# Performance work log

Hardware: AMD Instinct MI355X
Metric: run time of the kernel (lower is better)

The kernel has to match this reference:

```python
import jax, jax.numpy as jnp
import numpy as np

L = 4          # num_blocks
D = 256        # emb_dim
H = 8          # num_heads
DH = D         # per-head dim == emb_dim (module quirk: inner_dim = emb_dim * num_heads)
INNER = D * H  # 2048
M = 1024       # mlp_dim
EPS = 1e-5
SCALE = D ** (-0.5)


def layernorm(x, g, b):
    mu = jnp.mean(x, axis=-1, keepdims=True)
    var = jnp.mean(jnp.square(x - mu), axis=-1, keepdims=True)
    return (x - mu) * jax.lax.rsqrt(var + EPS) * g + b


def setup_inputs() -> dict:
    key = jax.random.key(0)
    ks = jax.random.split(key, 12)
    B, N = 8, 1024
    s = lambda fan: 1.0 / np.sqrt(fan)
    return {
        "inputs": jax.random.normal(ks[0], (B, N, D), dtype=jnp.float32),
        "ln1_g": jnp.ones((L, D), jnp.float32),
        "ln1_b": jnp.zeros((L, D), jnp.float32),
        "w_qkv": jax.random.normal(ks[1], (L, D, 3 * INNER), jnp.float32) * s(D),
        "w_proj": jax.random.normal(ks[2], (L, INNER, D), jnp.float32) * s(INNER),
        "b_proj": jnp.zeros((L, D), jnp.float32),
        "ln2_g": jnp.ones((L, D), jnp.float32),
        "ln2_b": jnp.zeros((L, D), jnp.float32),
        "w1": jax.random.normal(ks[3], (L, D, M), jnp.float32) * s(D),
        "b1": jnp.zeros((L, M), jnp.float32),
        "w2": jax.random.normal(ks[4], (L, M, D), jnp.float32) * s(M),
        "b2": jnp.zeros((L, D), jnp.float32),
    }


def attention(x, w_qkv, w_proj, b_proj):
    B, N, _ = x.shape
    qkv = x @ w_qkv                                  # [B, N, 3*INNER]
    q, k, v = jnp.split(qkv, 3, axis=-1)
    reshape = lambda t: t.reshape(B, N, H, DH).transpose(0, 2, 1, 3)  # b h n d
    q, k, v = reshape(q), reshape(k), reshape(v)
    dots = jnp.einsum("bhnd,bhmd->bhnm", q, k) * SCALE
    attn = jax.nn.softmax(dots, axis=-1)
    out = jnp.einsum("bhnm,bhmd->bhnd", attn, v)     # [B, H, N, DH]
    out = out.transpose(0, 2, 1, 3).reshape(B, N, INNER)
    return out @ w_proj + b_proj


def reference(inputs, ln1_g, ln1_b, w_qkv, w_proj, b_proj, ln2_g, ln2_b, w1, b1, w2, b2):
    x = inputs
    for l in range(L):
        # pre-LN multi-head attention + residual
        h = layernorm(x, ln1_g[l], ln1_b[l])
        x = x + attention(h, w_qkv[l], w_proj[l], b_proj[l])
        # pre-LN GELU MLP + residual (exact erf GELU, matching nn.GELU default)
        h = layernorm(x, ln2_g[l], ln2_b[l])
        h = jax.nn.gelu(h @ w1[l] + b1[l], approximate=False)
        x = x + (h @ w2[l] + b2[l])
    return x
```

## Files before the change

kernel.cpp:

```cpp
#include <hip/hip_runtime.h>
#include <math.h>

#define L_ 4
#define D_ 256
#define H_ 8
#define INNER_ 2048
#define M_ 1024
#define B_ 8
#define N_ 1024
#define R_ (B_ * N_)
#define QS_ 6144

constexpr float EPS_ = 1e-5f;
constexpr float SCALE_ = 0.0625f;

using f16 = _Float16;
typedef _Float16 f16x8 __attribute__((ext_vector_type(8)));
typedef float f32x4 __attribute__((ext_vector_type(4)));

__device__ __forceinline__ float gelu_f(float x) {
    return 0.5f * x * (1.0f + erff(x * 0.70710678118654752f));
}

__global__ __launch_bounds__(256)
void ln_kernel(const float* __restrict__ x, const float* __restrict__ g,
               const float* __restrict__ b, f16* __restrict__ out) {
    const int row = blockIdx.x;
    const int t = threadIdx.x;
    const int wave = t >> 6, lane = t & 63;
    __shared__ float red[8];

    const float v = x[(size_t)row * D_ + t];

    float s = v;
    #pragma unroll
    for (int o = 32; o; o >>= 1) s += __shfl_down(s, o);
    if (lane == 0) red[wave] = s;
    __syncthreads();
    const float mean = (red[0] + red[1] + red[2] + red[3]) * (1.0f / 256.0f);

    const float d = v - mean;
    float s2 = d * d;
    #pragma unroll
    for (int o = 32; o; o >>= 1) s2 += __shfl_down(s2, o);
    if (lane == 0) red[4 + wave] = s2;
    __syncthreads();
    const float var = (red[4] + red[5] + red[6] + red[7]) * (1.0f / 256.0f);

    out[(size_t)row * D_ + t] = (f16)(d * rsqrtf(var + EPS_) * g[t] + b[t]);
}

__global__ __launch_bounds__(256)
void transpose_w(const float* __restrict__ W, f16* __restrict__ Wt, int K, int N) {
    __shared__ float tile[64][68];
    const int n0 = blockIdx.x * 64, k0 = blockIdx.y * 64;
    const float* Wl = W + (size_t)blockIdx.z * K * N;
    f16* Wtl = Wt + (size_t)blockIdx.z * K * N;
    const int t = threadIdx.x;

    #pragma unroll
    for (int j = 0; j < 4; ++j) {
        const int li = t + 256 * j;
        const int r = li >> 4, c4 = (li & 15) * 4;
        const float4 v = *reinterpret_cast<const float4*>(&Wl[(size_t)(k0 + r) * N + n0 + c4]);
        tile[r][c4] = v.x; tile[r][c4 + 1] = v.y; tile[r][c4 + 2] = v.z; tile[r][c4 + 3] = v.w;
    }
    __syncthreads();
    #pragma unroll
    for (int j = 0; j < 2; ++j) {
        const int li = t + 256 * j;
        const int n = li >> 3, c8 = (li & 7) * 8;
        f16 tmp[8];
        #pragma unroll
        for (int e = 0; e < 8; ++e) tmp[e] = (f16)tile[c8 + e][n];
        *reinterpret_cast<uint4*>(&Wtl[(size_t)(n0 + n) * K + k0 + c8]) =
            *reinterpret_cast<const uint4*>(tmp);
    }
}

__global__ __launch_bounds__(256)
void transpose_v(const f16* __restrict__ qkv, f16* __restrict__ Vt) {
    __shared__ f16 tile[64][72];
    const int n0 = blockIdx.x * 64;
    const int d0 = blockIdx.y * 64;
    const int b = blockIdx.z;
    const int t = threadIdx.x;
    const f16* Vg = qkv + (size_t)b * N_ * QS_ + 4096;

    #pragma unroll
    for (int j = 0; j < 2; ++j) {
        const int li = t + 256 * j;
        const int r = li >> 3, c8 = (li & 7) * 8;
        *reinterpret_cast<uint4*>(&tile[r][c8]) =
            *reinterpret_cast<const uint4*>(&Vg[(size_t)(n0 + r) * QS_ + d0 + c8]);
    }
    __syncthreads();
    #pragma unroll
    for (int j = 0; j < 2; ++j) {
        const int li = t + 256 * j;
        const int dr = li >> 3, c8 = (li & 7) * 8;
        f16 tmp[8];
        #pragma unroll
        for (int e = 0; e < 8; ++e) tmp[e] = tile[c8 + e][dr];
        *reinterpret_cast<uint4*>(&Vt[((size_t)b * INNER_ + d0 + dr) * N_ + n0 + c8]) =
            *reinterpret_cast<const uint4*>(tmp);
    }
}

template <int WM, int WN, bool BIAS, bool RES, bool GELU, bool OUTF16>
__global__ __launch_bounds__(256)
void gemm_f16(const f16* __restrict__ A, int lda, const f16* __restrict__ Wt,
              const float* __restrict__ bias, f16* __restrict__ Cf16,
              float* __restrict__ Cf32, int ldc, int K) {
    constexpr int BM = 2 * WM, BN = 2 * WN, MI = WM / 16, NI = WN / 16;
    __shared__ uint4 As[BM * 8];
    __shared__ uint4 Bs[BN * 8];

    const int t = threadIdx.x;
    const int lane = t & 63, w = t >> 6;
    const int wr = w >> 1, wc = w & 1;
    const int row0 = blockIdx.y * BM, col0 = blockIdx.x * BN;
    const int l15 = lane & 15, l4 = lane >> 4;

    f32x4 acc[MI][NI];
    #pragma unroll
    for (int mi = 0; mi < MI; ++mi)
        #pragma unroll
        for (int ni = 0; ni < NI; ++ni) acc[mi][ni] = (f32x4){0.f, 0.f, 0.f, 0.f};

    for (int k0 = 0; k0 < K; k0 += 64) {
        #pragma unroll
        for (int j = 0; j < BM / 32; ++j) {
            const int ci = t + 256 * j, r = ci >> 3, c = ci & 7;
            As[r * 8 + (c ^ (r & 7))] =
                *reinterpret_cast<const uint4*>(&A[(size_t)(row0 + r) * lda + k0 + c * 8]);
        }
        #pragma unroll
        for (int j = 0; j < BN / 32; ++j) {
            const int ci = t + 256 * j, r = ci >> 3, c = ci & 7;
            Bs[r * 8 + (c ^ (r & 7))] =
                *reinterpret_cast<const uint4*>(&Wt[(size_t)(col0 + r) * K + k0 + c * 8]);
        }
        __syncthreads();

        #pragma unroll
        for (int tk = 0; tk < 2; ++tk) {
            f16x8 af[MI], bf[NI];
            #pragma unroll
            for (int mi = 0; mi < MI; ++mi) {
                const int r = wr * WM + mi * 16 + l15;
                af[mi] = *reinterpret_cast<const f16x8*>(&As[r * 8 + ((tk * 4 + l4) ^ (r & 7))]);
            }
            #pragma unroll
            for (int ni = 0; ni < NI; ++ni) {
                const int r = wc * WN + ni * 16 + l15;
                bf[ni] = *reinterpret_cast<const f16x8*>(&Bs[r * 8 + ((tk * 4 + l4) ^ (r & 7))]);
            }
            #pragma unroll
            for (int mi = 0; mi < MI; ++mi)
                #pragma unroll
                for (int ni = 0; ni < NI; ++ni)
                    acc[mi][ni] = __builtin_amdgcn_mfma_f32_16x16x32_f16(
                        af[mi], bf[ni], acc[mi][ni], 0, 0, 0);
        }
        __syncthreads();
    }

    #pragma unroll
    for (int mi = 0; mi < MI; ++mi) {
        #pragma unroll
        for (int ni = 0; ni < NI; ++ni) {
            const int col = col0 + wc * WN + ni * 16 + l15;
            float bv = 0.f;
            if constexpr (BIAS) bv = bias[col];
            #pragma unroll
            for (int r = 0; r < 4; ++r) {
                const size_t row = row0 + wr * WM + mi * 16 + l4 * 4 + r;
                float v = acc[mi][ni][r] + bv;
                if constexpr (GELU) v = gelu_f(v);
                if constexpr (OUTF16) {
                    Cf16[row * ldc + col] = (f16)v;
                } else {
                    float* p = &Cf32[row * ldc + col];
                    *p = RES ? (*p + v) : v;
                }
            }
        }
    }
}

__global__ __launch_bounds__(512, 1)
void attn_f16(f16* __restrict__ qkv, const f16* __restrict__ Vt) {
    __shared__ uint4 lds[9216];
    f16* Ps = (f16*)(lds + 8192);

    const int t = threadIdx.x, lane = t & 63, w = t >> 6;
    const int l15 = lane & 15, l4 = lane >> 4;
    const int lin = blockIdx.x;
    const int hh = lin & 7;
    const int q0 = ((lin >> 3) & 7) << 7;
    const int b = lin >> 6;

    f16* Qg = qkv + (size_t)b * N_ * QS_ + hh * 256;
    const f16* Kg = Qg + 2048;
    const f16* Vtg = Vt + ((size_t)b * INNER_ + hh * 256) * N_;

    uint4 qreg[8];
    #pragma unroll
    for (int j = 0; j < 8; ++j) {
        const int ci = t + 512 * j, r = ci >> 5, c = ci & 31;
        qreg[j] = *reinterpret_cast<const uint4*>(&Qg[(size_t)(q0 + r) * QS_ + c * 8]);
    }
    uint4 kreg[4], vreg[4];
    #pragma unroll
    for (int j = 0; j < 4; ++j) {
        const int ci = t + 512 * j, r = ci >> 5, c = ci & 31;
        kreg[j] = *reinterpret_cast<const uint4*>(&Kg[(size_t)r * QS_ + c * 8]);
    }
    #pragma unroll
    for (int j = 0; j < 4; ++j) {
        const int ci = t + 512 * j, r = ci >> 3, c = ci & 7;
        vreg[j] = *reinterpret_cast<const uint4*>(&Vtg[(size_t)r * N_ + c * 8]);
    }
    #pragma unroll
    for (int j = 0; j < 8; ++j) {
        const int ci = t + 512 * j, r = ci >> 5, c = ci & 31;
        lds[r * 32 + (c ^ (r & 7))] = qreg[j];
    }
    __syncthreads();
    f16x8 qf[8];
    {
        const int r = w * 16 + l15;
        #pragma unroll
        for (int tk = 0; tk < 8; ++tk)
            qf[tk] = *reinterpret_cast<const f16x8*>(&lds[r * 32 + ((tk * 4 + l4) ^ (r & 7))]);
    }
    __syncthreads();

    float m_run[4] = {-INFINITY, -INFINITY, -INFINITY, -INFINITY};
    float l_run[4] = {0.f, 0.f, 0.f, 0.f};
    f32x4 outf[16];
    #pragma unroll
    for (int f = 0; f < 16; ++f) outf[f] = (f32x4){0.f, 0.f, 0.f, 0.f};

    for (int kt = 0; kt < 16; ++kt) {
        uint4* Kc = (kt & 1) ? (lds + 2048) : lds;
        uint4* Vc = (kt & 1) ? (lds + 6144) : (lds + 4096);

        #pragma unroll
        for (int j = 0; j < 4; ++j) {
            const int ci = t + 512 * j, r = ci >> 5, c = ci & 31;
            Kc[r * 32 + (c ^ (r & 7))] = kreg[j];
        }
        #pragma unroll
        for (int j = 0; j < 4; ++j) {
            const int ci = t + 512 * j, r = ci >> 3, c = ci & 7;
            Vc[r * 8 + (c ^ (r & 7))] = vreg[j];
        }
        if (kt < 15) {
            const int kv0n = (kt + 1) * 64;
            #pragma unroll
            for (int j = 0; j < 4; ++j) {
                const int ci = t + 512 * j, r = ci >> 5, c = ci & 31;
                kreg[j] = *reinterpret_cast<const uint4*>(
                    &Kg[(size_t)(kv0n + r) * QS_ + c * 8]);
            }
            #pragma unroll
            for (int j = 0; j < 4; ++j) {
                const int ci = t + 512 * j, r = ci >> 3, c = ci & 7;
                vreg[j] = *reinterpret_cast<const uint4*>(
                    &Vtg[(size_t)r * N_ + kv0n + c * 8]);
            }
        }
        __syncthreads();

        f32x4 sf[4];
        #pragma unroll
        for (int nf = 0; nf < 4; ++nf) sf[nf] = (f32x4){0.f, 0.f, 0.f, 0.f};
        __builtin_amdgcn_s_setprio(1);
        #pragma unroll
        for (int tk = 0; tk < 8; ++tk) {
            #pragma unroll
            for (int nf = 0; nf < 4; ++nf) {
                const int r = nf * 16 + l15;
                const f16x8 bf =
                    *reinterpret_cast<const f16x8*>(&Kc[r * 32 + ((tk * 4 + l4) ^ (r & 7))]);
                sf[nf] = __builtin_amdgcn_mfma_f32_16x16x32_f16(qf[tk], bf, sf[nf], 0, 0, 0);
            }
        }
        __builtin_amdgcn_s_setprio(0);

        float mx[4], al[4], ps[4], p[4][4];
        #pragma unroll
        for (int r = 0; r < 4; ++r) {
            float v0 = sf[0][r] * SCALE_, v1 = sf[1][r] * SCALE_;
            float v2 = sf[2][r] * SCALE_, v3 = sf[3][r] * SCALE_;
            p[0][r] = v0; p[1][r] = v1; p[2][r] = v2; p[3][r] = v3;
            mx[r] = fmaxf(fmaxf(v0, v1), fmaxf(v2, v3));
        }
        #pragma unroll
        for (int off = 1; off < 16; off <<= 1)
            #pragma unroll
            for (int r = 0; r < 4; ++r) mx[r] = fmaxf(mx[r], __shfl_xor(mx[r], off));
        #pragma unroll
        for (int r = 0; r < 4; ++r) {
            const float nm = fmaxf(m_run[r], mx[r]);
            al[r] = __expf(m_run[r] - nm);
            m_run[r] = nm;
            float sum = 0.f;
            #pragma unroll
            for (int nf = 0; nf < 4; ++nf) {
                p[nf][r] = __expf(p[nf][r] - nm);
                sum += p[nf][r];
            }
            ps[r] = sum;
        }
        #pragma unroll
        for (int off = 1; off < 16; off <<= 1)
            #pragma unroll
            for (int r = 0; r < 4; ++r) ps[r] += __shfl_xor(ps[r], off);
        #pragma unroll
        for (int r = 0; r < 4; ++r) {
            l_run[r] = l_run[r] * al[r] + ps[r];
            const int q = w * 16 + l4 * 4 + r;
            #pragma unroll
            for (int nf = 0; nf < 4; ++nf) {
                const int kv = nf * 16 + l15;
                Ps[q * 64 + (kv ^ ((q & 7) << 3))] = (f16)p[nf][r];
            }
        }
        #pragma unroll
        for (int f = 0; f < 16; ++f)
            #pragma unroll
            for (int r = 0; r < 4; ++r) outf[f][r] *= al[r];

        __builtin_amdgcn_s_setprio(1);
        #pragma unroll
        for (int tk = 0; tk < 2; ++tk) {
            const int rq = w * 16 + l15;
            const int c = tk * 4 + l4;
            const f16x8 pa =
                *reinterpret_cast<const f16x8*>(&Ps[rq * 64 + ((c ^ (rq & 7)) * 8)]);
            #pragma unroll
            for (int f = 0; f < 16; ++f) {
                const int d = f * 16 + l15;
                const f16x8 vf = *reinterpret_cast<const f16x8*>(&Vc[d * 8 + (c ^ (d & 7))]);
                outf[f] = __builtin_amdgcn_mfma_f32_16x16x32_f16(pa, vf, outf[f], 0, 0, 0);
            }
        }
        __builtin_amdgcn_s_setprio(0);
    }

    __syncthreads();
    constexpr int OST = 272;
    f16* Os = (f16*)lds;
    float inv[4];
    #pragma unroll
    for (int r = 0; r < 4; ++r) inv[r] = 1.0f / l_run[r];
    #pragma unroll
    for (int f = 0; f < 16; ++f) {
        const int d = f * 16 + l15;
        #pragma unroll
        for (int r = 0; r < 4; ++r) {
            const int q = w * 16 + l4 * 4 + r;
            Os[q * OST + d] = (f16)(outf[f][r] * inv[r]);
        }
    }
    __syncthreads();
    #pragma unroll
    for (int j = 0; j < 8; ++j) {
        const int id = t + 512 * j;
        const int row = id >> 5, cc = id & 31;
        *reinterpret_cast<uint4*>(&Qg[(size_t)(q0 + row) * QS_ + cc * 8]) =
            *reinterpret_cast<const uint4*>(&Os[row * OST + cc * 8]);
    }
}

extern "C" void kernel_launch(void* const* d_in, const int* in_sizes, int n_in,
                              void* d_out, int out_size, void* d_ws, size_t ws_size,
                              hipStream_t stream) {
    (void)in_sizes; (void)n_in; (void)out_size;

    const float* inputs = (const float*)d_in[0];
    const float* ln1_g  = (const float*)d_in[1];
    const float* ln1_b  = (const float*)d_in[2];
    const float* w_qkv  = (const float*)d_in[3];
    const float* w_proj = (const float*)d_in[4];
    const float* b_proj = (const float*)d_in[5];
    const float* ln2_g  = (const float*)d_in[6];
    const float* ln2_b  = (const float*)d_in[7];
    const float* w1     = (const float*)d_in[8];
    const float* b1     = (const float*)d_in[9];
    const float* w2     = (const float*)d_in[10];
    const float* b2     = (const float*)d_in[11];

    float* x = (float*)d_out;

    f16* ws = (f16*)d_ws;
    const size_t SZ_WQKV = (size_t)L_ * D_ * 3 * INNER_;
    const size_t SZ_WPRJ = (size_t)L_ * INNER_ * D_;
    const size_t SZ_W1   = (size_t)L_ * D_ * M_;
    const size_t SZ_W2   = (size_t)L_ * M_ * D_;
    const size_t SZ_H    = (size_t)R_ * D_;
    f16* wt_qkv = ws;
    f16* wt_prj = wt_qkv + SZ_WQKV;
    f16* wt1    = wt_prj + SZ_WPRJ;
    f16* wt2    = wt1 + SZ_W1;
    f16* h      = wt2 + SZ_W2;
    f16* qc     = h + SZ_H;

    const size_t fixed = SZ_WQKV + SZ_WPRJ + SZ_W1 + SZ_W2 + SZ_H;
    int nch = 1;
    while (nch < 8 &&
           2 * (fixed + ((size_t)R_ / nch) * (QS_ + INNER_)) > ws_size)
        nch *= 2;
    const int CB = B_ / nch;
    const int CR = R_ / nch;
    f16* vt = qc + (size_t)CR * QS_;

    hipMemcpyAsync(x, inputs, (size_t)R_ * D_ * sizeof(float),
                   hipMemcpyDeviceToDevice, stream);

    transpose_w<<<dim3(96, 4, L_), 256, 0, stream>>>(w_qkv, wt_qkv, D_, 3 * INNER_);
    transpose_w<<<dim3(4, 32, L_), 256, 0, stream>>>(w_proj, wt_prj, INNER_, D_);
    transpose_w<<<dim3(16, 4, L_), 256, 0, stream>>>(w1, wt1, D_, M_);
    transpose_w<<<dim3(4, 16, L_), 256, 0, stream>>>(w2, wt2, M_, D_);

    for (int l = 0; l < L_; ++l) {
        ln_kernel<<<R_, 256, 0, stream>>>(x, ln1_g + l * D_, ln1_b + l * D_, h);

        for (int c = 0; c < nch; ++c) {
            const size_t r0 = (size_t)c * CR;
            gemm_f16<64, 64, false, false, false, true>
                <<<dim3(QS_ / 128, CR / 128), 256, 0, stream>>>(
                    h + r0 * D_, D_, wt_qkv + (size_t)l * D_ * 3 * INNER_,
                    nullptr, qc, nullptr, QS_, D_);

            transpose_v<<<dim3(16, 32, CB), 256, 0, stream>>>(qc, vt);

            attn_f16<<<(N_ / 128) * H_ * CB, 512, 0, stream>>>(qc, vt);

            gemm_f16<32, 32, true, true, false, false>
                <<<dim3(D_ / 64, CR / 64), 256, 0, stream>>>(
                    qc, QS_, wt_prj + (size_t)l * INNER_ * D_,
                    b_proj + l * D_, nullptr, x + r0 * D_, D_, INNER_);
        }

        ln_kernel<<<R_, 256, 0, stream>>>(x, ln2_g + l * D_, ln2_b + l * D_, h);

        for (int c = 0; c < nch; ++c) {
            const size_t r0 = (size_t)c * CR;
            f16* hid = qc;
            gemm_f16<64, 64, true, false, true, true>
                <<<dim3(M_ / 128, CR / 128), 256, 0, stream>>>(
                    h + r0 * D_, D_, wt1 + (size_t)l * D_ * M_,
                    b1 + l * M_, hid, nullptr, M_, D_);

            gemm_f16<32, 32, true, true, false, false>
                <<<dim3(D_ / 64, CR / 64), 256, 0, stream>>>(
                    hid, M_, wt2 + (size_t)l * M_ * D_,
                    b2 + l * D_, nullptr, x + r0 * D_, D_, M_);
        }
    }
}
```

Before: 1.654 ms.

## Restructure attention kernel with direct global-to-LDS loads and 2 m-tiles per wave

Rewrites the flash-attention kernel to use 256 threads with each wave handling two 16-row query tiles, sharing K fragments across both tiles. K/V tiles shrink to 32 keys and are streamed with global_load_lds directly into double-buffered LDS, replacing register staging. Row sums are computed with an MFMA against a ones vector instead of shuffle reductions. The launch bounds allow two blocks per CU for occupancy. The costs are twice as many loop iterations, each carrying a block-wide barrier, and roughly doubled accumulator register pressure.

```diff
diff --git a/kernel.cpp b/kernel.cpp
--- a/kernel.cpp
+++ b/kernel.cpp
@@ -20,6 +20,12 @@
 
 __device__ __forceinline__ float gelu_f(float x) {
     return 0.5f * x * (1.0f + erff(x * 0.70710678118654752f));
+}
+
+__device__ __forceinline__ void gll16(const f16* src, f16* dst) {
+    __builtin_amdgcn_global_load_lds(
+        (const __attribute__((address_space(1))) unsigned int*)src,
+        (__attribute__((address_space(3))) unsigned int*)dst, 16, 0, 0);
 }
 
 __global__ __launch_bounds__(256)
@@ -189,10 +195,10 @@
     }
 }
 
-__global__ __launch_bounds__(512, 1)
+__global__ __launch_bounds__(256, 2)
 void attn_f16(f16* __restrict__ qkv, const f16* __restrict__ Vt) {
-    __shared__ uint4 lds[9216];
-    f16* Ps = (f16*)(lds + 8192);
+    __shared__ alignas(16) f16 lds[36864];
+    f16* const Ps = lds + 32768;
 
     const int t = threadIdx.x, lane = t & 63, w = t >> 6;
     const int l15 = lane & 15, l4 = lane >> 4;
@@ -205,147 +211,166 @@
     const f16* Kg = Qg + 2048;
     const f16* Vtg = Vt + ((size_t)b * INNER_ + hh * 256) * N_;
 
-    uint4 qreg[8];
-    #pragma unroll
-    for (int j = 0; j < 8; ++j) {
-        const int ci = t + 512 * j, r = ci >> 5, c = ci & 31;
-        qreg[j] = *reinterpret_cast<const uint4*>(&Qg[(size_t)(q0 + r) * QS_ + c * 8]);
-    }
-    uint4 kreg[4], vreg[4];
-    #pragma unroll
-    for (int j = 0; j < 4; ++j) {
-        const int ci = t + 512 * j, r = ci >> 5, c = ci & 31;
-        kreg[j] = *reinterpret_cast<const uint4*>(&Kg[(size_t)r * QS_ + c * 8]);
-    }
-    #pragma unroll
-    for (int j = 0; j < 4; ++j) {
-        const int ci = t + 512 * j, r = ci >> 3, c = ci & 7;
-        vreg[j] = *reinterpret_cast<const uint4*>(&Vtg[(size_t)r * N_ + c * 8]);
-    }
-    #pragma unroll
-    for (int j = 0; j < 8; ++j) {
-        const int ci = t + 512 * j, r = ci >> 5, c = ci & 31;
-        lds[r * 32 + (c ^ (r & 7))] = qreg[j];
-    }
-    __syncthreads();
-    f16x8 qf[8];
+    #pragma unroll
+    for (int j = 0; j < 32; ++j) {
+        const int cb = (j * 4 + w) << 6;
+        const int ci = cb + lane;
+        const int r = ci >> 5, c = ci & 31;
+        gll16(Qg + (size_t)(q0 + r) * QS_ + ((c ^ (r & 7)) << 3), lds + cb * 8);
+    }
+    __syncthreads();
+    f16x8 qf[2][8];
+    #pragma unroll
+    for (int mi = 0; mi < 2; ++mi) {
+        const int q = w * 32 + mi * 16 + l15;
+        #pragma unroll
+        for (int tk = 0; tk < 8; ++tk) {
+            const int cc = tk * 4 + l4;
+            qf[mi][tk] = *reinterpret_cast<const f16x8*>(
+                lds + q * 256 + ((cc ^ (q & 7)) << 3));
+        }
+    }
+    __syncthreads();
+
     {
-        const int r = w * 16 + l15;
-        #pragma unroll
-        for (int tk = 0; tk < 8; ++tk)
-            qf[tk] = *reinterpret_cast<const f16x8*>(&lds[r * 32 + ((tk * 4 + l4) ^ (r & 7))]);
-    }
-    __syncthreads();
-
-    float m_run[4] = {-INFINITY, -INFINITY, -INFINITY, -INFINITY};
-    float l_run[4] = {0.f, 0.f, 0.f, 0.f};
-    f32x4 outf[16];
-    #pragma unroll
-    for (int f = 0; f < 16; ++f) outf[f] = (f32x4){0.f, 0.f, 0.f, 0.f};
-
-    for (int kt = 0; kt < 16; ++kt) {
-        uint4* Kc = (kt & 1) ? (lds + 2048) : lds;
-        uint4* Vc = (kt & 1) ? (lds + 6144) : (lds + 4096);
-
         #pragma unroll
         for (int j = 0; j < 4; ++j) {
-            const int ci = t + 512 * j, r = ci >> 5, c = ci & 31;
-            Kc[r * 32 + (c ^ (r & 7))] = kreg[j];
+            const int cb = (j * 4 + w) << 6, ci = cb + lane;
+            const int r = ci >> 5, c = ci & 31;
+            gll16(Kg + (size_t)r * QS_ + ((c ^ (r & 7)) << 3), lds + cb * 8);
         }
         #pragma unroll
         for (int j = 0; j < 4; ++j) {
-            const int ci = t + 512 * j, r = ci >> 3, c = ci & 7;
-            Vc[r * 8 + (c ^ (r & 7))] = vreg[j];
-        }
-        if (kt < 15) {
-            const int kv0n = (kt + 1) * 64;
+            const int cb = (j * 4 + w) << 6, ci = cb + lane;
+            const int d = ci >> 2, c = ci & 3;
+            gll16(Vtg + (size_t)d * N_ + ((c ^ (d & 3)) << 3), lds + 16384 + cb * 8);
+        }
+    }
+
+    const f16x8 kOnes = {(f16)1, (f16)1, (f16)1, (f16)1,
+                         (f16)1, (f16)1, (f16)1, (f16)1};
+    float m_run[2][4];
+    #pragma unroll
+    for (int mi = 0; mi < 2; ++mi)
+        #pragma unroll
+        for (int r = 0; r < 4; ++r) m_run[mi][r] = -INFINITY;
+    f32x4 outf[2][16];
+    f32x4 sums[2];
+    #pragma unroll
+    for (int mi = 0; mi < 2; ++mi) {
+        sums[mi] = (f32x4){0.f, 0.f, 0.f, 0.f};
+        #pragma unroll
+        for (int f = 0; f < 16; ++f) outf[mi][f] = (f32x4){0.f, 0.f, 0.f, 0.f};
+    }
+
+    for (int kt = 0; kt < 32; ++kt) {
+        f16* const Kc = (kt & 1) ? (lds + 8192) : lds;
+        f16* const Vc = (kt & 1) ? (lds + 24576) : (lds + 16384);
+        __syncthreads();
+
+        if (kt < 31) {
+            const int kv0 = (kt + 1) * 32;
+            f16* const Kn = (kt & 1) ? lds : (lds + 8192);
+            f16* const Vn = (kt & 1) ? (lds + 16384) : (lds + 24576);
             #pragma unroll
             for (int j = 0; j < 4; ++j) {
-                const int ci = t + 512 * j, r = ci >> 5, c = ci & 31;
-                kreg[j] = *reinterpret_cast<const uint4*>(
-                    &Kg[(size_t)(kv0n + r) * QS_ + c * 8]);
+                const int cb = (j * 4 + w) << 6, ci = cb + lane;
+                const int r = ci >> 5, c = ci & 31;
+                gll16(Kg + (size_t)(kv0 + r) * QS_ + ((c ^ (r & 7)) << 3), Kn + cb * 8);
             }
             #pragma unroll
             for (int j = 0; j < 4; ++j) {
-                const int ci = t + 512 * j, r = ci >> 3, c = ci & 7;
-                vreg[j] = *reinterpret_cast<const uint4*>(
-                    &Vtg[(size_t)r * N_ + kv0n + c * 8]);
-            }
-        }
-        __syncthreads();
-
-        f32x4 sf[4];
-        #pragma unroll
-        for (int nf = 0; nf < 4; ++nf) sf[nf] = (f32x4){0.f, 0.f, 0.f, 0.f};
+                const int cb = (j * 4 + w) << 6, ci = cb + lane;
+                const int d = ci >> 2, c = ci & 3;
+                gll16(Vtg + (size_t)d * N_ + kv0 + ((c ^ (d & 3)) << 3), Vn + cb * 8);
+            }
+        }
+
+        f32x4 sf[2][2];
+        #pragma unroll
+        for (int mi = 0; mi < 2; ++mi)
+            #pragma unroll
+            for (int nf = 0; nf < 2; ++nf) sf[mi][nf] = (f32x4){0.f, 0.f, 0.f, 0.f};
         __builtin_amdgcn_s_setprio(1);
         #pragma unroll
         for (int tk = 0; tk < 8; ++tk) {
             #pragma unroll
-            for (int nf = 0; nf < 4; ++nf) {
+            for (int nf = 0; nf < 2; ++nf) {
                 const int r = nf * 16 + l15;
-                const f16x8 bf =
-                    *reinterpret_cast<const f16x8*>(&Kc[r * 32 + ((tk * 4 + l4) ^ (r & 7))]);
-                sf[nf] = __builtin_amdgcn_mfma_f32_16x16x32_f16(qf[tk], bf, sf[nf], 0, 0, 0);
+                const int cc = tk * 4 + l4;
+                const f16x8 bf = *reinterpret_cast<const f16x8*>(
+                    Kc + r * 256 + ((cc ^ (r & 7)) << 3));
+                #pragma unroll
+                for (int mi = 0; mi < 2; ++mi)
+                    sf[mi][nf] = __builtin_amdgcn_mfma_f32_16x16x32_f16(
+                        qf[mi][tk], bf, sf[mi][nf], 0, 0, 0);
             }
         }
         __builtin_amdgcn_s_setprio(0);
 
-        float mx[4], al[4], ps[4], p[4][4];
-        #pragma unroll
-        for (int r = 0; r < 4; ++r) {
-            float v0 = sf[0][r] * SCALE_, v1 = sf[1][r] * SCALE_;
-            float v2 = sf[2][r] * SCALE_, v3 = sf[3][r] * SCALE_;
-            p[0][r] = v0; p[1][r] = v1; p[2][r] = v2; p[3][r] = v3;
-            mx[r] = fmaxf(fmaxf(v0, v1), fmaxf(v2, v3));
-        }
+        float mx[2][4], al[2][4], p[2][2][4];
+        #pragma unroll
+        for (int mi = 0; mi < 2; ++mi)
+            #pragma unroll
+            for (int r = 0; r < 4; ++r) {
+                const float v0 = sf[mi][0][r] * SCALE_;
+                const float v1 = sf[mi][1][r] * SCALE_;
+                p[mi][0][r] = v0; p[mi][1][r] = v1;
+                mx[mi][r] = fmaxf(v0, v1);
+            }
         #pragma unroll
         for (int off = 1; off < 16; off <<= 1)
             #pragma unroll
-            for (int r = 0; r < 4; ++r) mx[r] = fmaxf(mx[r], __shfl_xor(mx[r], off));
-        #pragma unroll
-        for (int r = 0; r < 4; ++r) {
-            const float nm = fmaxf(m_run[r], mx[r]);
-            al[r] = __expf(m_run[r] - nm);
-            m_run[r] = nm;
-            float sum = 0.f;
-            #pragma unroll
-            for (int nf = 0; nf < 4; ++nf) {
-                p[nf][r] = __expf(p[nf][r] - nm);
-                sum += p[nf][r];
-            }
-            ps[r] = sum;
-        }
-        #pragma unroll
-        for (int off = 1; off < 16; off <<= 1)
-            #pragma unroll
-            for (int r = 0; r < 4; ++r) ps[r] += __shfl_xor(ps[r], off);
-        #pragma unroll
-        for (int r = 0; r < 4; ++r) {
-            l_run[r] = l_run[r] * al[r] + ps[r];
-            const int q = w * 16 + l4 * 4 + r;
-            #pragma unroll
-            for (int nf = 0; nf < 4; ++nf) {
-                const int kv = nf * 16 + l15;
-                Ps[q * 64 + (kv ^ ((q & 7) << 3))] = (f16)p[nf][r];
-            }
-        }
-        #pragma unroll
-        for (int f = 0; f < 16; ++f)
-            #pragma unroll
-            for (int r = 0; r < 4; ++r) outf[f][r] *= al[r];
+            for (int mi = 0; mi < 2; ++mi)
+                #pragma unroll
+                for (int r = 0; r < 4; ++r)
+                    mx[mi][r] = fmaxf(mx[mi][r], __shfl_xor(mx[mi][r], off));
+        #pragma unroll
+        for (int mi = 0; mi < 2; ++mi)
+            #pragma unroll
+            for (int r = 0; r < 4; ++r) {
+                const float nm = fmaxf(m_run[mi][r], mx[mi][r]);
+                al[mi][r] = __expf(m_run[mi][r] - nm);
+                m_run[mi][r] = nm;
+                p[mi][0][r] = __expf(p[mi][0][r] - nm);
+                p[mi][1][r] = __expf(p[mi][1][r] - nm);
+            }
+        #pragma unroll
+        for (int mi = 0; mi < 2; ++mi)
+            #pragma unroll
+            for (int r = 0; r < 4; ++r) {
+                const int q = w * 32 + mi * 16 + l4 * 4 + r;
+                #pragma unroll
+                for (int nf = 0; nf < 2; ++nf) {
+                    const int kv = nf * 16 + l15;
+                    Ps[q * 32 + (((kv >> 3) ^ (q & 3)) << 3) + (kv & 7)] =
+                        (f16)p[mi][nf][r];
+                }
+            }
+        #pragma unroll
+        for (int mi = 0; mi < 2; ++mi) {
+            #pragma unroll
+            for (int r = 0; r < 4; ++r) sums[mi][r] *= al[mi][r];
+            #pragma unroll
+            for (int f = 0; f < 16; ++f)
+                #pragma unroll
+                for (int r = 0; r < 4; ++r) outf[mi][f][r] *= al[mi][r];
+        }
 
         __builtin_amdgcn_s_setprio(1);
         #pragma unroll
-        for (int tk = 0; tk < 2; ++tk) {
-            const int rq = w * 16 + l15;
-            const int c = tk * 4 + l4;
-            const f16x8 pa =
-                *reinterpret_cast<const f16x8*>(&Ps[rq * 64 + ((c ^ (rq & 7)) * 8)]);
+        for (int mi = 0; mi < 2; ++mi) {
+            const int q = w * 32 + mi * 16 + l15;
+            const f16x8 pa = *reinterpret_cast<const f16x8*>(
+                Ps + q * 32 + ((l4 ^ (q & 3)) << 3));
+            sums[mi] = __builtin_amdgcn_mfma_f32_16x16x32_f16(pa, kOnes, sums[mi], 0, 0, 0);
             #pragma unroll
             for (int f = 0; f < 16; ++f) {
                 const int d = f * 16 + l15;
-                const f16x8 vf = *reinterpret_cast<const f16x8*>(&Vc[d * 8 + (c ^ (d & 7))]);
-                outf[f] = __builtin_amdgcn_mfma_f32_16x16x32_f16(pa, vf, outf[f], 0, 0, 0);
+                const f16x8 vf = *reinterpret_cast<const f16x8*>(
+                    Vc + d * 32 + ((l4 ^ (d & 3)) << 3));
+                outf[mi][f] = __builtin_amdgcn_mfma_f32_16x16x32_f16(
+                    pa, vf, outf[mi][f], 0, 0, 0);
             }
         }
         __builtin_amdgcn_s_setprio(0);
@@ -353,23 +378,27 @@
 
     __syncthreads();
     constexpr int OST = 272;
-    f16* Os = (f16*)lds;
-    float inv[4];
-    #pragma unroll
-    for (int r = 0; r < 4; ++r) inv[r] = 1.0f / l_run[r];
-    #pragma unroll
-    for (int f = 0; f < 16; ++f) {
-        const int d = f * 16 + l15;
-        #pragma unroll
-        for (int r = 0; r < 4; ++r) {
-            const int q = w * 16 + l4 * 4 + r;
-            Os[q * OST + d] = (f16)(outf[f][r] * inv[r]);
-        }
-    }
-    __syncthreads();
-    #pragma unroll
-    for (int j = 0; j < 8; ++j) {
-        const int id = t + 512 * j;
+    f16* Os = lds;
+    float inv[2][4];
+    #pragma unroll
+    for (int mi = 0; mi < 2; ++mi)
+        #pragma unroll
+        for (int r = 0; r < 4; ++r) inv[mi][r] = 1.0f / sums[mi][r];
+    #pragma unroll
+    for (int mi = 0; mi < 2; ++mi)
+        #pragma unroll
+        for (int f = 0; f < 16; ++f) {
+            const int d = f * 16 + l15;
+            #pragma unroll
+            for (int r = 0; r < 4; ++r) {
+                const int q = w * 32 + mi * 16 + l4 * 4 + r;
+                Os[q * OST + d] = (f16)(outf[mi][f][r] * inv[mi][r]);
+            }
+        }
+    __syncthreads();
+    #pragma unroll
+    for (int j = 0; j < 16; ++j) {
+        const int id = t + 256 * j;
         const int row = id >> 5, cc = id & 31;
         *reinterpret_cast<uint4*>(&Qg[(size_t)(q0 + row) * QS_ + cc * 8]) =
             *reinterpret_cast<const uint4*>(&Os[row * OST + cc * 8]);
@@ -438,7 +467,7 @@
 
             transpose_v<<<dim3(16, 32, CB), 256, 0, stream>>>(qc, vt);
 
-            attn_f16<<<(N_ / 128) * H_ * CB, 512, 0, stream>>>(qc, vt);
+            attn_f16<<<(N_ / 128) * H_ * CB, 256, 0, stream>>>(qc, vt);
 
             gemm_f16<32, 32, true, true, false, false>
                 <<<dim3(D_ / 64, CR / 64), 256, 0, stream>>>(
```

Measured after the change: 1.728 ms. 4.4% more time.
